# Performance work log

Measured on AMD Instinct MI355X. Metric: run time of the kernel, lower is better.

Reference implementation:

```python
import jax, jax.numpy as jnp
import numpy as np

B, C, H, W = 64, 256, 64, 64


def setup_inputs() -> dict:
    key = jax.random.key(0)
    k1, k2, k3 = jax.random.split(key, 3)
    inp = jax.random.normal(k1, (B, C, H, W), dtype=jnp.float32)
    action_out = jax.random.normal(k2, (B, 9), dtype=jnp.float32)
    std = 1.0 / (C * 9)
    conv_weight = jax.random.uniform(k3, (C, C, 3, 3), dtype=jnp.float32,
                                     minval=-std, maxval=std)
    return {"inp": inp, "action_out": action_out, "conv_weight": conv_weight}


def _conv_one(x, w):
    # x: [C, H, W], w: [C, C, 3, 3] -> [C, H, W], padding=1 (SAME for 3x3)
    y = jax.lax.conv_general_dilated(
        x[None], w, window_strides=(1, 1), padding=((1, 1), (1, 1)),
        dimension_numbers=("NCHW", "OIHW", "NCHW"))
    return y[0]


def reference(inp, action_out, conv_weight):
    # per-sample softmax mask over the 9 kernel taps
    mask = jax.nn.softmax(action_out, axis=-1).reshape(-1, 1, 1, 3, 3)  # [B,1,1,3,3]
    weight_b = mask * conv_weight[None]  # [B, C, C, 3, 3]
    out = jax.vmap(_conv_one)(inp, weight_b)  # batched per-sample conv
    return out
```

## Files before the change

kernel.cpp:

```cpp
#include <hip/hip_runtime.h>
#include <hip/hip_bf16.h>
#include <stdint.h>
#include <math.h>


typedef __hip_bfloat16 bf16;
using frag_ab = __attribute__((ext_vector_type(8))) short;
using frag_cd = __attribute__((ext_vector_type(4))) float;

#define AS1 __attribute__((address_space(1)))
#define AS3 __attribute__((address_space(3)))

#define NB 64
#define NC 256
#define NH 64
#define NW 64
#define HP 66
#define WP 66
#define KTOT 2304
#define XP_ELEMS ((size_t)NB * HP * WP * NC)
#define WT_ELEMS ((size_t)NC * KTOT)

#define BS_OFF 65536
#define RS_OFF 131136
#define SMEM_BYTES 131200

__device__ __forceinline__ void gld_lds16(const void* g, void* l) {
    __builtin_amdgcn_global_load_lds((const AS1 void*)g, (AS3 void*)l, 16, 0, 0);
}

__global__ __launch_bounds__(256) void wt_kernel(const float* __restrict__ w,
                                                 bf16* __restrict__ Wt) {
    int o = blockIdx.x;
    int t = threadIdx.x;
    __shared__ alignas(16) bf16 buf[KTOT];
    #pragma unroll
    for (int j = 0; j < 9; j++) {
        int idx = j * 256 + t;
        float v = w[(size_t)o * KTOT + idx];
        int i = idx / 9, tap = idx - i * 9;
        buf[tap * 256 + i] = __float2bfloat16(v);
    }
    __syncthreads();
    const uint4* s = (const uint4*)buf;
    uint4* dst = (uint4*)(Wt + (size_t)o * KTOT);
    dst[t] = s[t];
    if (t < 32) dst[256 + t] = s[256 + t];
}

__global__ __launch_bounds__(256) void border_kernel(bf16* __restrict__ Xp) {
    int id = blockIdx.x * 256 + threadIdx.x;
    int ch = id & 31;
    int px = (id >> 5) % 260;
    int b  = (id >> 5) / 260;
    int y, x;
    if (px < 66)       { y = 0;  x = px; }
    else if (px < 132) { y = 65; x = px - 66; }
    else { int e = px - 132; y = 1 + (e >> 1); x = (e & 1) * 65; }
    bf16* dst = Xp + (((size_t)b * HP + y) * WP + x) * NC + ch * 8;
    uint4 z; z.x = 0; z.y = 0; z.z = 0; z.w = 0;
    *(uint4*)dst = z;
}

__global__ __launch_bounds__(256) void pad_kernel(const float* __restrict__ inp,
                                                  bf16* __restrict__ Xp) {
    int bid = blockIdx.x;
    int cb = bid & 3;
    int y  = (bid >> 2) & 63;
    int b  = bid >> 8;
    __shared__ bf16 tile[64][66];
    int t = threadIdx.x;
    int xp = (t & 31) * 2, tr = t >> 5;
    const float* src = inp + (((size_t)b * NC + cb * 64) * NH + y) * NW + xp;
    #pragma unroll
    for (int ci = 0; ci < 4; ci++) {
        int c = tr * 8 + ci * 2;
        float2 v0 = *(const float2*)(src + (size_t)c * (NH * NW));
        float2 v1 = *(const float2*)(src + (size_t)(c + 1) * (NH * NW));
        union { bf16 h[2]; uint u; } p0, p1;
        p0.h[0] = __float2bfloat16(v0.x); p0.h[1] = __float2bfloat16(v1.x);
        p1.h[0] = __float2bfloat16(v0.y); p1.h[1] = __float2bfloat16(v1.y);
        *(uint*)&tile[xp][c]     = p0.u;
        *(uint*)&tile[xp + 1][c] = p1.u;
    }
    __syncthreads();
    #pragma unroll
    for (int pp = 0; pp < 2; pp++) {
        int x = pp * 32 + (t >> 3);
        int s = t & 7;
        uint u0 = *(const uint*)&tile[x][s * 8 + 0];
        uint u1 = *(const uint*)&tile[x][s * 8 + 2];
        uint u2 = *(const uint*)&tile[x][s * 8 + 4];
        uint u3 = *(const uint*)&tile[x][s * 8 + 6];
        uint4 val; val.x = u0; val.y = u1; val.z = u2; val.w = u3;
        bf16* dst = Xp + (((size_t)b * HP + (y + 1)) * WP + (x + 1)) * NC + cb * 64 + s * 8;
        *(uint4*)dst = val;
    }
}

__global__ __launch_bounds__(512, 2) void gemm_kernel(const bf16* __restrict__ Wt,
                                                      const float* __restrict__ act,
                                                      const bf16* __restrict__ Xp,
                                                      float* __restrict__ out) {
    extern __shared__ char sm[];

    int bid = blockIdx.x;
    int wg = (bid & 7) * 128 + (bid >> 3);
    int b  = wg >> 4;
    int nt = wg & 15;
    int ybase = nt * 4;

    int tid = threadIdx.x;
    int w = tid >> 6, l = tid & 63;
    int wm = w >> 2, wn = w & 3;
    int lm = l & 15, lq = l >> 4;

    if (tid == 0) {
        float m[9], mx = -1e30f;
        #pragma unroll
        for (int i = 0; i < 9; i++) { m[i] = act[b * 9 + i]; mx = fmaxf(mx, m[i]); }
        float s = 0.f;
        #pragma unroll
        for (int i = 0; i < 9; i++) { m[i] = expf(m[i] - mx); s += m[i]; }
        float inv = 1.f / s;
        #pragma unroll
        for (int i = 0; i < 9; i++) m[i] *= inv;
        float* rs = (float*)(sm + RS_OFF);
        #pragma unroll
        for (int i = 1; i < 9; i++) rs[i] = m[i - 1] / m[i];
        rs[9] = m[8];
    }

    int pA0 = ((lq + (lm & 7)) & 7) * 16;
    int pA1 = ((lq + 4 + (lm & 7)) & 7) * 16;
    int aRdRow = (wm * 128 + lm) * 128;
    int bRdRow = (wn * 64 + lm) * 128;

    int qs = ((l & 7) - (l >> 3)) & 7;
    int qe = qs * 8;
    int srcAf[2], srcAb[2], srcBf[2], srcBb[2];
    int dAf[2], dAb[2], dBf[2], dBb[2];
    #pragma unroll
    for (int r = 0; r < 2; r++) {
        int j  = w * 16 + r * 8 + (l >> 3);
        int j0 = w * 16 + r * 8;
        int RAf = j  + ((j  < 64) ? 0 : 64);
        int R0f = j0 + ((j0 < 64) ? 0 : 64);
        int RAb = j  + ((j  < 64) ? 64 : 128);
        int R0b = j0 + ((j0 < 64) ? 64 : 128);
        srcAf[r] = RAf * KTOT + qe;
        srcAb[r] = RAb * KTOT + qe;
        dAf[r] = R0f * 128;
        dAb[r] = R0b * 128;
        int pixf  = ((j  >> 5) << 6) + (j  & 31);
        int pix0f = ((j0 >> 5) << 6) + (j0 & 31);
        srcBf[r] = ((b * HP + ybase + (pixf >> 6)) * WP + (pixf & 63)) * NC + qe;
        dBf[r] = BS_OFF + pix0f * 128;
        int pixb = pixf + 32;
        srcBb[r] = ((b * HP + ybase + (pixb >> 6)) * WP + (pixb & 63)) * NC + qe;
        dBb[r] = BS_OFF + (pix0f + 32) * 128;
    }

#define STAGE_A_F(SAE, BUFN) { _Pragma("unroll") for (int r = 0; r < 2; r++) \
    gld_lds16(Wt + srcAf[r] + (SAE), sm + (BUFN) * 32768 + dAf[r]); }
#define STAGE_A_B(SAE, BUFN) { _Pragma("unroll") for (int r = 0; r < 2; r++) \
    gld_lds16(Wt + srcAb[r] + (SAE), sm + (BUFN) * 32768 + dAb[r]); }
#define STAGE_B_F(SBE, BUFN) { _Pragma("unroll") for (int r = 0; r < 2; r++) \
    gld_lds16(Xp + srcBf[r] + (SBE), sm + (BUFN) * 32768 + dBf[r]); }
#define STAGE_B_B(SBE, BUFN) { _Pragma("unroll") for (int r = 0; r < 2; r++) \
    gld_lds16(Xp + srcBb[r] + (SBE), sm + (BUFN) * 32768 + dBb[r]); }

    STAGE_A_F(0, 0);
    __builtin_amdgcn_sched_barrier(0);
    STAGE_B_F(0, 0);
    __builtin_amdgcn_sched_barrier(0);
    STAGE_B_B(0, 0);
    __builtin_amdgcn_sched_barrier(0);
    STAGE_A_B(0, 0);
    asm volatile("s_waitcnt lgkmcnt(0)" ::: "memory");
    asm volatile("s_waitcnt vmcnt(4)" ::: "memory");
    __builtin_amdgcn_s_barrier();

    frag_cd acc[8][4];
    #pragma unroll
    for (int i = 0; i < 8; i++)
        #pragma unroll
        for (int jx = 0; jx < 4; jx++)
            #pragma unroll
            for (int q = 0; q < 4; q++) acc[i][jx][q] = 0.f;

    frag_ab af[2][4], bfr[2][2];

#define LD_A(MH) { _Pragma("unroll") for (int mf = 0; mf < 4; mf++) { \
    af[0][mf] = *(const frag_ab*)(aB0 + (MH) * 8192 + mf * 2048); \
    af[1][mf] = *(const frag_ab*)(aB1 + (MH) * 8192 + mf * 2048); } }
#define LD_B(NHH) { _Pragma("unroll") for (int nf = 0; nf < 2; nf++) { \
    bfr[0][nf] = *(const frag_ab*)(bB0 + (NHH) * 4096 + nf * 2048); \
    bfr[1][nf] = *(const frag_ab*)(bB1 + (NHH) * 4096 + nf * 2048); } }
#define MM(MH, NHH) { __builtin_amdgcn_s_setprio(1); \
    _Pragma("unroll") for (int mf = 0; mf < 4; mf++) \
    _Pragma("unroll") for (int nf = 0; nf < 2; nf++) { \
        acc[(MH)*4+mf][(NHH)*2+nf] = __builtin_amdgcn_mfma_f32_16x16x32_bf16( \
            af[0][mf], bfr[0][nf], acc[(MH)*4+mf][(NHH)*2+nf], 0, 0, 0); \
        acc[(MH)*4+mf][(NHH)*2+nf] = __builtin_amdgcn_mfma_f32_16x16x32_bf16( \
            af[1][mf], bfr[1][nf], acc[(MH)*4+mf][(NHH)*2+nf], 0, 0, 0); } \
    __builtin_amdgcn_s_setprio(0); }

    #pragma unroll 1
    for (int t = 0; t < 35; ++t) {
        int buf = t & 1, bufN = buf ^ 1;
        if ((t & 3) == 0 && t) {
            float rsc = *(const float*)(sm + RS_OFF + (t >> 2) * 4);
            #pragma unroll
            for (int i = 0; i < 8; i++)
                #pragma unroll
                for (int jx = 0; jx < 4; jx++)
                    #pragma unroll
                    for (int q = 0; q < 4; q++) acc[i][jx][q] *= rsc;
        }
        int tn = t + 1;
        int sAe = tn * 64;
        int tapN = tn >> 2;
        int dyN = tapN / 3, dxN = tapN - 3 * dyN;
        int sBe = (dyN * WP + dxN) * NC + (tn & 3) * 64;

        const char* aB0 = sm + buf * 32768 + aRdRow + pA0;
        const char* aB1 = sm + buf * 32768 + aRdRow + pA1;
        const char* bB0 = sm + buf * 32768 + bRdRow + pA0;
        const char* bB1 = sm + buf * 32768 + bRdRow + pA1;
        bB0 += BS_OFF; bB1 += BS_OFF;

        LD_A(0); LD_B(0);
        STAGE_A_F(sAe, bufN);
        MM(0, 0);
        __builtin_amdgcn_sched_barrier(0);
        asm volatile("s_waitcnt vmcnt(4)" ::: "memory");
        __builtin_amdgcn_s_barrier();

        LD_B(1);
        STAGE_B_F(sBe, bufN);
        MM(0, 1);
        __builtin_amdgcn_sched_barrier(0);
        asm volatile("s_waitcnt vmcnt(4)" ::: "memory");
        __builtin_amdgcn_s_barrier();

        LD_A(1);
        STAGE_B_B(sBe, bufN);
        MM(1, 1);
        __builtin_amdgcn_sched_barrier(0);

        LD_B(0);
        STAGE_A_B(sAe, bufN);
        MM(1, 0);
        __builtin_amdgcn_sched_barrier(0);
        asm volatile("s_waitcnt vmcnt(4)" ::: "memory");
        __builtin_amdgcn_s_barrier();
    }

    {
        const char* aB0 = sm + 32768 + aRdRow + pA0;
        const char* aB1 = sm + 32768 + aRdRow + pA1;
        const char* bB0 = sm + 32768 + bRdRow + pA0 + BS_OFF;
        const char* bB1 = sm + 32768 + bRdRow + pA1 + BS_OFF;

        LD_A(0); LD_B(0);
        MM(0, 0);
        __builtin_amdgcn_sched_barrier(0);
        asm volatile("s_waitcnt vmcnt(2)" ::: "memory");
        __builtin_amdgcn_s_barrier();

        LD_B(1);
        MM(0, 1);
        __builtin_amdgcn_sched_barrier(0);
        asm volatile("s_waitcnt vmcnt(0)" ::: "memory");
        __builtin_amdgcn_s_barrier();

        LD_A(1);
        MM(1, 1);
        __builtin_amdgcn_sched_barrier(0);

        LD_B(0);
        MM(1, 0);
    }

    float m8 = *(const float*)(sm + RS_OFF + 9 * 4);
    int rqBase = lq * 4;
    #pragma unroll
    for (int mh = 0; mh < 2; mh++)
        #pragma unroll
        for (int mf = 0; mf < 4; mf++)
            #pragma unroll
            for (int nh = 0; nh < 2; nh++)
                #pragma unroll
                for (int nf = 0; nf < 2; nf++) {
                    int m = wm * 128 + mh * 64 + mf * 16 + rqBase;
                    int n = nt * 256 + wn * 64 + nh * 32 + nf * 16 + lm;
                    float* po = out + ((size_t)(b * 256 + m)) * 4096 + n;
                    frag_cd v = acc[mh * 4 + mf][nh * 2 + nf];
                    #pragma unroll
                    for (int q = 0; q < 4; q++) po[(size_t)q * 4096] = m8 * v[q];
                }
}

__global__ void diag_kernel(float* out) { out[threadIdx.x] = 12345.0f; }

extern "C" void kernel_launch(void* const* d_in, const int* in_sizes, int n_in,
                              void* d_out, int out_size, void* d_ws, size_t ws_size,
                              hipStream_t stream) {
    const float* inp = (const float*)d_in[0];
    const float* act = (const float*)d_in[1];
    const float* wgt = (const float*)d_in[2];
    float* out = (float*)d_out;

    size_t WT_OFF = 0;
    size_t XP_OFF = WT_ELEMS * sizeof(bf16);
    size_t NEED  = XP_OFF + XP_ELEMS * sizeof(bf16);

    if (ws_size < NEED) {
        diag_kernel<<<1, 256, 0, stream>>>(out);
        return;
    }

    bf16* Wt = (bf16*)((char*)d_ws + WT_OFF);
    bf16* Xp = (bf16*)((char*)d_ws + XP_OFF);

    hipFuncSetAttribute((const void*)gemm_kernel,
                        hipFuncAttributeMaxDynamicSharedMemorySize, SMEM_BYTES);

    wt_kernel<<<NC, 256, 0, stream>>>(wgt, Wt);
    border_kernel<<<(NB * 260 * 32) / 256, 256, 0, stream>>>(Xp);
    pad_kernel<<<NB * NH * 4, 256, 0, stream>>>(inp, Xp);
    gemm_kernel<<<NB * 16, 512, SMEM_BYTES, stream>>>(Wt, act, Xp, out);
}
```

Baseline: 700.6 us.

## Deepen LDS prefetch to two stages ahead and refill buffers in place

Global-to-LDS staging now runs two K-steps ahead instead of one. Both buffers are filled in the prologue. Each iteration refills the buffer it is consuming, after the matching fragments have been read, with barriers between phases. B fragments for both N-halves are held in separate register sets, so all B reads happen at the start of the step. The goal is to hide global load latency better behind the MFMA work. The cost is more VGPRs, more in-flight loads (vmcnt 8), and a tricky overwrite-while-reading ordering that could race if the half-buffer regions overlap.

New measurement: 695.9 us. Within noise of the previous version (-0.7%).

```diff
diff --git a/kernel.cpp b/kernel.cpp
--- a/kernel.cpp
+++ b/kernel.cpp
@@ -170,15 +170,14 @@
 #define STAGE_B_B(SBE, BUFN) { _Pragma("unroll") for (int r = 0; r < 2; r++) \
     gld_lds16(Xp + srcBb[r] + (SBE), sm + (BUFN) * 32768 + dBb[r]); }
 
-    STAGE_A_F(0, 0);
-    __builtin_amdgcn_sched_barrier(0);
-    STAGE_B_F(0, 0);
-    __builtin_amdgcn_sched_barrier(0);
-    STAGE_B_B(0, 0);
-    __builtin_amdgcn_sched_barrier(0);
-    STAGE_A_B(0, 0);
+    {
+        STAGE_A_F(0, 0); STAGE_B_F(0, 0); STAGE_B_B(0, 0); STAGE_A_B(0, 0);
+        __builtin_amdgcn_sched_barrier(0);
+        int sBe1 = 64;
+        STAGE_A_F(64, 1); STAGE_B_F(sBe1, 1); STAGE_B_B(sBe1, 1); STAGE_A_B(64, 1);
+    }
     asm volatile("s_waitcnt lgkmcnt(0)" ::: "memory");
-    asm volatile("s_waitcnt vmcnt(4)" ::: "memory");
+    asm volatile("s_waitcnt vmcnt(8)" ::: "memory");
     __builtin_amdgcn_s_barrier();
 
     frag_cd acc[8][4];
@@ -189,26 +188,26 @@
             #pragma unroll
             for (int q = 0; q < 4; q++) acc[i][jx][q] = 0.f;
 
-    frag_ab af[2][4], bfr[2][2];
+    frag_ab af[2][4], bfr0[2][2], bfr1[2][2];
 
 #define LD_A(MH) { _Pragma("unroll") for (int mf = 0; mf < 4; mf++) { \
     af[0][mf] = *(const frag_ab*)(aB0 + (MH) * 8192 + mf * 2048); \
     af[1][mf] = *(const frag_ab*)(aB1 + (MH) * 8192 + mf * 2048); } }
-#define LD_B(NHH) { _Pragma("unroll") for (int nf = 0; nf < 2; nf++) { \
-    bfr[0][nf] = *(const frag_ab*)(bB0 + (NHH) * 4096 + nf * 2048); \
-    bfr[1][nf] = *(const frag_ab*)(bB1 + (NHH) * 4096 + nf * 2048); } }
-#define MM(MH, NHH) { __builtin_amdgcn_s_setprio(1); \
+#define LD_B_TO(BFA, NHH) { _Pragma("unroll") for (int nf = 0; nf < 2; nf++) { \
+    BFA[0][nf] = *(const frag_ab*)(bB0 + (NHH) * 4096 + nf * 2048); \
+    BFA[1][nf] = *(const frag_ab*)(bB1 + (NHH) * 4096 + nf * 2048); } }
+#define MM(MH, NHH, BFA) { __builtin_amdgcn_s_setprio(1); \
     _Pragma("unroll") for (int mf = 0; mf < 4; mf++) \
     _Pragma("unroll") for (int nf = 0; nf < 2; nf++) { \
         acc[(MH)*4+mf][(NHH)*2+nf] = __builtin_amdgcn_mfma_f32_16x16x32_bf16( \
-            af[0][mf], bfr[0][nf], acc[(MH)*4+mf][(NHH)*2+nf], 0, 0, 0); \
+            af[0][mf], BFA[0][nf], acc[(MH)*4+mf][(NHH)*2+nf], 0, 0, 0); \
         acc[(MH)*4+mf][(NHH)*2+nf] = __builtin_amdgcn_mfma_f32_16x16x32_bf16( \
-            af[1][mf], bfr[1][nf], acc[(MH)*4+mf][(NHH)*2+nf], 0, 0, 0); } \
+            af[1][mf], BFA[1][nf], acc[(MH)*4+mf][(NHH)*2+nf], 0, 0, 0); } \
     __builtin_amdgcn_s_setprio(0); }
 
     #pragma unroll 1
-    for (int t = 0; t < 35; ++t) {
-        int buf = t & 1, bufN = buf ^ 1;
+    for (int t = 0; t < 34; ++t) {
+        int buf = t & 1;
         if ((t & 3) == 0 && t) {
             float rsc = *(const float*)(sm + RS_OFF + (t >> 2) * 4);
             #pragma unroll
@@ -218,7 +217,7 @@
                     #pragma unroll
                     for (int q = 0; q < 4; q++) acc[i][jx][q] *= rsc;
         }
-        int tn = t + 1;
+        int tn = t + 2;
         int sAe = tn * 64;
         int tapN = tn >> 2;
         int dyN = tapN / 3, dxN = tapN - 3 * dyN;
@@ -226,61 +225,66 @@
 
         const char* aB0 = sm + buf * 32768 + aRdRow + pA0;
         const char* aB1 = sm + buf * 32768 + aRdRow + pA1;
-        const char* bB0 = sm + buf * 32768 + bRdRow + pA0;
-        const char* bB1 = sm + buf * 32768 + bRdRow + pA1;
-        bB0 += BS_OFF; bB1 += BS_OFF;
-
-        LD_A(0); LD_B(0);
-        STAGE_A_F(sAe, bufN);
-        MM(0, 0);
+        const char* bB0 = sm + buf * 32768 + bRdRow + pA0 + BS_OFF;
+        const char* bB1 = sm + buf * 32768 + bRdRow + pA1 + BS_OFF;
+
+        LD_A(0); LD_B_TO(bfr0, 0); LD_B_TO(bfr1, 1);
+        MM(0, 0, bfr0);
+        __builtin_amdgcn_sched_barrier(0);
+        __builtin_amdgcn_s_barrier();
+
+        MM(0, 1, bfr1);
+        STAGE_A_F(sAe, buf); STAGE_B_F(sBe, buf);
+        __builtin_amdgcn_sched_barrier(0);
+        __builtin_amdgcn_s_barrier();
+
+        LD_A(1);
+        MM(1, 1, bfr1);
+        STAGE_B_B(sBe, buf);
+        __builtin_amdgcn_sched_barrier(0);
+        __builtin_amdgcn_s_barrier();
+
+        MM(1, 0, bfr0);
+        STAGE_A_B(sAe, buf);
+        __builtin_amdgcn_sched_barrier(0);
+        asm volatile("s_waitcnt vmcnt(8)" ::: "memory");
+        __builtin_amdgcn_s_barrier();
+    }
+
+
+    {
+        const char* aB0 = sm + 0 * 32768 + aRdRow + pA0;
+        const char* aB1 = sm + 0 * 32768 + aRdRow + pA1;
+        const char* bB0 = sm + 0 * 32768 + bRdRow + pA0 + BS_OFF;
+        const char* bB1 = sm + 0 * 32768 + bRdRow + pA1 + BS_OFF;
+        LD_A(0); LD_B_TO(bfr0, 0); LD_B_TO(bfr1, 1);
+        MM(0, 0, bfr0);
+        MM(0, 1, bfr1);
+        LD_A(1);
+        MM(1, 1, bfr1);
+        MM(1, 0, bfr0);
         __builtin_amdgcn_sched_barrier(0);
         asm volatile("s_waitcnt vmcnt(4)" ::: "memory");
         __builtin_amdgcn_s_barrier();
-
-        LD_B(1);
-        STAGE_B_F(sBe, bufN);
-        MM(0, 1);
-        __builtin_amdgcn_sched_barrier(0);
-        asm volatile("s_waitcnt vmcnt(4)" ::: "memory");
-        __builtin_amdgcn_s_barrier();
-
+    }
+    {
+        const char* aB0 = sm + 1 * 32768 + aRdRow + pA0;
+        const char* aB1 = sm + 1 * 32768 + aRdRow + pA1;
+        const char* bB0 = sm + 1 * 32768 + bRdRow + pA0 + BS_OFF;
+        const char* bB1 = sm + 1 * 32768 + bRdRow + pA1 + BS_OFF;
+        LD_A(0); LD_B_TO(bfr0, 0);
+        MM(0, 0, bfr0);
+        __builtin_amdgcn_sched_barrier(0);
+        asm volatile("s_waitcnt vmcnt(2)" ::: "memory");
+        __builtin_amdgcn_s_barrier();
+        LD_B_TO(bfr1, 1);
+        MM(0, 1, bfr1);
+        __builtin_amdgcn_sched_barrier(0);
+        asm volatile("s_waitcnt vmcnt(0)" ::: "memory");
+        __builtin_amdgcn_s_barrier();
         LD_A(1);
-        STAGE_B_B(sBe, bufN);
-        MM(1, 1);
-        __builtin_amdgcn_sched_barrier(0);
-
-        LD_B(0);
-        STAGE_A_B(sAe, bufN);
-        MM(1, 0);
-        __builtin_amdgcn_sched_barrier(0);
-        asm volatile("s_waitcnt vmcnt(4)" ::: "memory");
-        __builtin_amdgcn_s_barrier();
-    }
-
-    {
-        const char* aB0 = sm + 32768 + aRdRow + pA0;
-        const char* aB1 = sm + 32768 + aRdRow + pA1;
-        const char* bB0 = sm + 32768 + bRdRow + pA0 + BS_OFF;
-        const char* bB1 = sm + 32768 + bRdRow + pA1 + BS_OFF;
-
-        LD_A(0); LD_B(0);
-        MM(0, 0);
-        __builtin_amdgcn_sched_barrier(0);
-        asm volatile("s_waitcnt vmcnt(2)" ::: "memory");
-        __builtin_amdgcn_s_barrier();
-
-        LD_B(1);
-        MM(0, 1);
-        __builtin_amdgcn_sched_barrier(0);
-        asm volatile("s_waitcnt vmcnt(0)" ::: "memory");
-        __builtin_amdgcn_s_barrier();
-
-        LD_A(1);
-        MM(1, 1);
-        __builtin_amdgcn_sched_barrier(0);
-
-        LD_B(0);
-        MM(1, 0);
+        MM(1, 1, bfr1);
+        MM(1, 0, bfr0);
     }
 
     float m8 = *(const float*)(sm + RS_OFF + 9 * 4);
```
